# Optimization experiments

Hardware: AMD Instinct MI355X
Metric: run time of the kernel (lower is better)

## Reference

```python
import jax, jax.numpy as jnp
import numpy as np
from jax import lax

P_BOX, N_PTS, K_MAX, HID, SAMP = 512, 50000, 64, 256, 4
C_IMG, HF, WF = 96, 160, 512
IMG_W, IMG_H = 1280.0, 384.0
OFFSET_SCALE = 0.04
PT_IN = 7


def _lin(key, fan_in, fan_out):
    return jax.random.normal(key, (fan_in, fan_out), dtype=jnp.float32) / np.sqrt(fan_in)


def setup_inputs() -> dict:
    key = jax.random.key(0)
    ks = jax.random.split(key, 24)
    xy = jax.random.uniform(ks[0], (N_PTS, 2), minval=-40.0, maxval=40.0)
    z = jax.random.uniform(ks[1], (N_PTS, 1), minval=-2.0, maxval=4.0)
    feats = jax.random.normal(ks[2], (N_PTS, 4))
    points = jnp.concatenate([xy, z, feats], axis=-1).astype(jnp.float32)
    ctr_xy = jax.random.uniform(ks[3], (P_BOX, 2), minval=-35.0, maxval=35.0)
    ctr_z = jax.random.uniform(ks[4], (P_BOX, 1), minval=-1.0, maxval=2.0)
    dxy = jax.random.uniform(ks[5], (P_BOX, 2), minval=2.0, maxval=6.0)
    dz = jax.random.uniform(ks[6], (P_BOX, 1), minval=1.0, maxval=3.0)
    yaw = jax.random.uniform(ks[7], (P_BOX, 1), minval=-np.pi, maxval=np.pi)
    boxes = jnp.concatenate([ctr_xy, ctr_z, dxy, dz, yaw], axis=-1).astype(jnp.float32)
    image_feat = jax.random.normal(ks[8], (1, C_IMG, HF, WF), dtype=jnp.float32)
    fx = fy = 400.0
    proj = jnp.array([[IMG_W / 2, -fx, 0.0, 0.0], [IMG_H / 2, 0.0, -fy, 0.0], [1.0, 0.0, 0.0, 0.0]], dtype=jnp.float32)
    return {
        'points': points, 'boxes': boxes, 'image_feat': image_feat, 'proj': proj,
        'pe_w1': _lin(ks[9], PT_IN + 1, HID), 'pe_b1': jnp.zeros((HID,), jnp.float32),
        'pe_w2': _lin(ks[10], HID, HID), 'pe_b2': jnp.zeros((HID,), jnp.float32),
        'q_w': _lin(ks[11], HID, HID), 'q_b': jnp.zeros((HID,), jnp.float32),
        'f_w': _lin(ks[12], C_IMG, HID), 'f_b': jnp.zeros((HID,), jnp.float32),
        'off_w': _lin(ks[13], HID, SAMP * 2), 'off_b': jnp.zeros((SAMP * 2,), jnp.float32),
        'wt_w': _lin(ks[14], HID, SAMP), 'wt_b': jnp.zeros((SAMP,), jnp.float32),
        'o_w1': _lin(ks[15], 2 * HID, HID), 'o_b1': jnp.zeros((HID,), jnp.float32),
        'o_w2': _lin(ks[16], HID, HID), 'o_b2': jnp.zeros((HID,), jnp.float32),
        'score_w': _lin(ks[17], HID, 1), 'score_b': jnp.zeros((1,), jnp.float32),
    }


def _fused_features(points, boxes, image_feat, proj, pe_w1, pe_b1, pe_w2, pe_b2,
                    q_w, q_b, f_w, f_b, off_w, off_b, wt_w, wt_b,
                    o_w1, o_b1, o_w2, o_b2, score_w, score_b):
    NEG = jnp.float32(-1e30)
    xyz = points[:, :3]
    ctr, dims, yaw = boxes[:, :3], boxes[:, 3:6], boxes[:, 6]
    c, s = jnp.cos(yaw)[:, None], jnp.sin(yaw)[:, None]
    rel = xyz[None, :, :] - ctr[:, None, :]                      # [P,N,3]
    lx = rel[..., 0] * c + rel[..., 1] * s                       # box-frame coords
    ly = -rel[..., 0] * s + rel[..., 1] * c
    lz = rel[..., 2]
    half = dims[:, None, :] * 0.5
    inside = (jnp.abs(lx) <= half[..., 0]) & (jnp.abs(ly) <= half[..., 1]) & (jnp.abs(lz) <= half[..., 2])
    counts = inside.sum(axis=1)                                  # [P]
    d = jnp.maximum(dims, 1e-3)[:, None, :]
    nx, ny, nz = lx / d[..., 0], ly / d[..., 1], lz / d[..., 2] - 0.5
    planar = jnp.where(inside, jnp.sqrt(nx * nx + ny * ny), jnp.inf)
    _, idx = lax.top_k(-planar, K_MAX)                           # K closest inside points
    slot_valid = jnp.arange(K_MAX)[None, :] < counts[:, None]    # [P,K]
    take = lambda a: jnp.take_along_axis(a, idx, axis=1)
    nl = jnp.stack([take(nx), take(ny), take(nz)], axis=-1)      # [P,K,3]
    nl = jnp.where(slot_valid[..., None], nl, 0.0)
    pts_sel = jnp.where(slot_valid[..., None], points[idx], 0.0)  # [P,K,7]
    # local density: knn(4) mean distance, excluding self
    diff = nl[:, :, None, :] - nl[:, None, :, :]
    dmat = jnp.sqrt((diff * diff).sum(-1) + 1e-12)               # [P,K,K]
    dmat = jnp.where(slot_valid[:, None, :], dmat, jnp.inf)
    knn = -lax.top_k(-dmat, 4)[0]                                # 4 smallest, col0 = self
    m = jnp.minimum(counts, K_MAX)
    col_ok = jnp.arange(1, 4)[None, None, :] < jnp.minimum(m, 4)[:, None, None]
    nb = jnp.where(col_ok, knn[:, :, 1:], 0.0)
    n_nb = jnp.maximum(jnp.minimum(m, 4) - 1, 1).astype(nl.dtype)
    density = jnp.where(slot_valid, jnp.exp(-nb.sum(-1) / n_nb[:, None]), 0.0)  # [P,K]
    tokens = jnp.concatenate([nl, pts_sel[:, :, 3:PT_IN], density[..., None]], axis=-1)  # [P,K,8]
    h = jnp.maximum(tokens @ pe_w1 + pe_b1, 0.0) @ pe_w2 + pe_b2  # point encoder [P,K,H]
    # project points to normalized image coords
    hom = pts_sel[:, :, :3] @ proj[:, :3].T + proj[:, 3]
    depth = hom[..., 2]
    safe_d = jnp.where(jnp.abs(depth) > 1e-3, depth, 1e-3)
    rx = 2.0 * (hom[..., 0] / safe_d) / (IMG_W - 1.0) - 1.0
    ry = 2.0 * (hom[..., 1] / safe_d) / (IMG_H - 1.0) - 1.0
    ref = jnp.stack([rx, ry], axis=-1)                           # [P,K,2]
    valid = (depth > 0.1) & (jnp.abs(rx) <= 1.0) & (jnp.abs(ry) <= 1.0) & slot_valid
    # cross-modal deformable attention (lite)
    q = h @ q_w + q_b
    fm = jnp.einsum('chw,cd->dhw', image_feat[0], f_w) + f_b[:, None, None]  # [H,Hf,Wf]
    offs = (jnp.tanh(h @ off_w + off_b)).reshape(P_BOX, K_MAX, SAMP, 2) * OFFSET_SCALE
    w = jax.nn.softmax(h @ wt_w + wt_b, axis=-1)                 # [P,K,S]
    grid = jnp.clip(ref[:, :, None, :] + offs, -1.2, 1.2)
    px = (grid[..., 0] + 1.0) * 0.5 * (WF - 1)                   # align_corners=True
    py = (grid[..., 1] + 1.0) * 0.5 * (HF - 1)
    x0, y0 = jnp.floor(px), jnp.floor(py)

    def gather(xi, yi):
        inb = (xi >= 0) & (xi <= WF - 1) & (yi >= 0) & (yi <= HF - 1)
        xc = jnp.clip(xi, 0, WF - 1).astype(jnp.int32)
        yc = jnp.clip(yi, 0, HF - 1).astype(jnp.int32)
        return fm[:, yc, xc] * inb[None].astype(fm.dtype)        # [H,P,K,S]

    wx1, wy1 = px - x0, py - y0
    samp = (gather(x0, y0) * (1 - wx1) * (1 - wy1) + gather(x0 + 1, y0) * wx1 * (1 - wy1)
            + gather(x0, y0 + 1) * (1 - wx1) * wy1 + gather(x0 + 1, y0 + 1) * wx1 * wy1)
    samp = jnp.moveaxis(samp, 0, -1)                             # [P,K,S,H]
    vm = valid.astype(h.dtype)
    samp = samp * vm[:, :, None, None]
    w = w * vm[:, :, None]
    w = w / jnp.maximum(w.sum(-1, keepdims=True), 1e-6)
    context = (samp * w[..., None]).sum(axis=2) * vm[..., None]  # [P,K,H]
    cat = jnp.concatenate([q * vm[..., None], context], axis=-1)
    img_tok = jnp.maximum(cat @ o_w1 + o_b1, 0.0) @ o_w2 + o_b2
    fused = h + img_tok                                          # [P,K,H]
    # masked attention pooling over valid slots
    logits = (fused @ score_w + score_b).squeeze(-1)
    logits = jnp.where(slot_valid, logits, NEG)
    valid_rows = slot_valid.any(axis=1)
    logits = jnp.where(valid_rows[:, None], logits, 0.0)
    pw = jnp.where(valid_rows[:, None], jax.nn.softmax(logits, axis=-1), 0.0)
    pooled = jnp.einsum('pk,pkd->pd', pw, fused)                 # [P,H]
    return pooled, counts.astype(jnp.float32)[:, None]


def reference(points, boxes, image_feat, proj, pe_w1, pe_b1, pe_w2, pe_b2,
              q_w, q_b, f_w, f_b, off_w, off_b, wt_w, wt_b,
              o_w1, o_b1, o_w2, o_b2, score_w, score_b):
    return _fused_features(points, boxes, image_feat, proj, pe_w1, pe_b1, pe_w2, pe_b2,
                           q_w, q_b, f_w, f_b, off_w, off_b, wt_w, wt_b,
                           o_w1, o_b1, o_w2, o_b2, score_w, score_b)
```

## Files before the change

### kernel.cpp

```cpp
#include <hip/hip_runtime.h>
#include <hip/hip_bf16.h>

#define P_BOX 512
#define NP    50000
#define NPAD  50176
#define KM    64
#define NKEY  4096
#define HF    160
#define WF    512

typedef unsigned long long u64;
typedef unsigned short u16;
typedef unsigned int u32;
typedef __attribute__((ext_vector_type(8))) short short8;
typedef __attribute__((ext_vector_type(4))) float f32x4;

__device__ __forceinline__ u16 f2bf(float f) {
  u32 u = __float_as_uint(f);
  u32 r = u + 0x7fffu + ((u >> 16) & 1u);
  return (u16)(r >> 16);
}
__device__ __forceinline__ float bf2f(u16 h) { return __uint_as_float(((u32)h) << 16); }
__device__ __forceinline__ float bfl(u32 u) { return __uint_as_float(u << 16); }
__device__ __forceinline__ float bfh(u32 u) { return __uint_as_float(u & 0xffff0000u); }

__device__ __forceinline__ int aIdx(int m, int d) {
  return m * 256 + (((d >> 3) ^ (m & 7)) << 3) + (d & 7);
}
__device__ __forceinline__ const short8* aGr(const u16* A, int m, int g) {
  return (const short8*)(A + m * 256 + ((g ^ (m & 7)) << 3));
}
__device__ __forceinline__ u16* aGrW(u16* A, int m, int g) {
  return A + m * 256 + ((g ^ (m & 7)) << 3);
}

__launch_bounds__(256, 4)
__global__ void k_prep(const float* __restrict__ pts,
                       const float* __restrict__ img,
                       const float* __restrict__ q_w, const float* __restrict__ q_b,
                       const float* __restrict__ f_w, const float* __restrict__ f_b,
                       const float* __restrict__ o_w1, const float* __restrict__ pe_w2,
                       const float* __restrict__ o_w2, const float* __restrict__ off_w,
                       const float* __restrict__ wt_w, const float* __restrict__ off_b,
                       const float* __restrict__ wt_b,
                       float* __restrict__ xs, float* __restrict__ ys, float* __restrict__ zs,
                       u16* __restrict__ pe_w2T, u16* __restrict__ WqT,
                       u16* __restrict__ o_w2T, u16* __restrict__ FoT,
                       u16* __restrict__ HWT, float* __restrict__ bq,
                       float* __restrict__ fbo, float* __restrict__ hb,
                       u16* __restrict__ imgT) {
  __shared__ float shbuf[8580];
  const int blk = blockIdx.x;
  const int t = threadIdx.x;

  if (blk < 24) {
    const bool isWq = blk < 16;
    const int g = isWq ? blk : blk - 16;
    const int n0 = (g & 3) * 64;
    const int x0 = (g >> 2) * 64;
    float* sA = shbuf;
    float* sB = shbuf + 64 * 65;
    float acc[4][4];
#pragma unroll
    for (int r = 0; r < 4; ++r)
#pragma unroll
      for (int c = 0; c < 4; ++c) acc[r][c] = 0.f;
    const int tx = t & 15, ty = t >> 4;
    for (int j0 = 0; j0 < 256; j0 += 64) {
      {
        int nn = t & 63;
        int jb = t >> 6;
#pragma unroll
        for (int r = 0; r < 16; ++r) {
          int jj = jb + r * 4;
          int row = (isWq ? 0 : 256) + j0 + jj;
          sA[jj * 65 + nn] = o_w1[row * 256 + n0 + nn];
        }
      }
      {
        int jj = t & 63;
        int xb = t >> 6;
#pragma unroll
        for (int r = 0; r < 16; ++r) {
          int xx = xb + r * 4;
          float v = 0.f;
          if (isWq) v = q_w[(x0 + xx) * 256 + j0 + jj];
          else if (x0 + xx < 96) v = f_w[(x0 + xx) * 256 + j0 + jj];
          sB[jj * 65 + xx] = v;
        }
      }
      __syncthreads();
#pragma unroll 8
      for (int jj = 0; jj < 64; ++jj) {
        float a[4], b[4];
#pragma unroll
        for (int r = 0; r < 4; ++r) a[r] = sA[jj * 65 + ty * 4 + r];
#pragma unroll
        for (int c = 0; c < 4; ++c) b[c] = sB[jj * 65 + tx * 4 + c];
#pragma unroll
        for (int r = 0; r < 4; ++r)
#pragma unroll
          for (int c = 0; c < 4; ++c) acc[r][c] += a[r] * b[c];
      }
      __syncthreads();
    }
    if (isWq) {
#pragma unroll
      for (int r = 0; r < 4; ++r) {
        ushort4 o;
        o.x = f2bf(acc[r][0]); o.y = f2bf(acc[r][1]);
        o.z = f2bf(acc[r][2]); o.w = f2bf(acc[r][3]);
        *(ushort4*)(WqT + (size_t)(n0 + ty * 4 + r) * 256 + x0 + tx * 4) = o;
      }
    } else {
      if (x0 + tx * 4 < 96) {
#pragma unroll
        for (int r = 0; r < 4; ++r) {
          ushort4 o;
          o.x = f2bf(acc[r][0]); o.y = f2bf(acc[r][1]);
          o.z = f2bf(acc[r][2]); o.w = f2bf(acc[r][3]);
          *(ushort4*)(FoT + (size_t)(n0 + ty * 4 + r) * 96 + x0 + tx * 4) = o;
        }
      }
    }
  } else if (blk < 56) {
    int g = blk - 24;
    const float* src = (g < 16) ? pe_w2 : o_w2;
    u16* dst = (g < 16) ? pe_w2T : o_w2T;
    int tile = g & 15;
    int n0 = (tile & 3) * 64, k0 = (tile >> 2) * 64;
    {
      int nn = t & 63, kb = t >> 6;
#pragma unroll
      for (int r = 0; r < 16; ++r) {
        int kk = kb + r * 4;
        shbuf[kk * 65 + nn] = src[(k0 + kk) * 256 + n0 + nn];
      }
    }
    __syncthreads();
    {
      int kk = t & 63, nb = t >> 6;
#pragma unroll
      for (int r = 0; r < 16; ++r) {
        int nn = nb + r * 4;
        dst[(size_t)(n0 + nn) * 256 + k0 + kk] = f2bf(shbuf[kk * 65 + nn]);
      }
    }
  } else if (blk == 56) {
    int n = t;
    float a1 = 0.f, a2 = 0.f;
    for (int j = 0; j < 256; ++j) {
      a1 += q_b[j] * o_w1[j * 256 + n];
      a2 += f_b[j] * o_w1[(256 + j) * 256 + n];
    }
    bq[n] = a1;
    fbo[n] = a2;
#pragma unroll
    for (int s = 0; s < 16; ++s) {
      float v = (s < 8) ? off_w[n * 8 + s] : ((s < 12) ? wt_w[n * 4 + (s - 8)] : 0.f);
      HWT[s * 256 + n] = f2bf(v);
    }
    if (t < 16) hb[t] = (t < 8) ? off_b[t] : ((t < 12) ? wt_b[t - 8] : 0.f);
  } else if (blk < 1337) {
    int g = blk - 57;
    int w0 = (g & 7) * 64;
    int h = g >> 3;
    int c0 = t >> 6, w = t & 63;
    for (int it = 0; it < 24; ++it) {
      int c = it * 4 + c0;
      shbuf[c * 65 + w] = img[(c * HF + h) * WF + w0 + w];
    }
    __syncthreads();
    for (int it = 0; it < 24; ++it) {
      int idx = it * 256 + t;
      int ww = idx / 96, c = idx % 96;
      imgT[((size_t)(h * WF + w0 + ww)) * 96 + c] = f2bf(shbuf[c * 65 + ww]);
    }
  } else {
    int g = blk - 1337;
#pragma unroll
    for (int r = 0; r < 4; ++r) {
      int i = g * 1024 + r * 256 + t;
      if (i < NPAD) {
        if (i < NP) {
          xs[i] = pts[i * 7 + 0];
          ys[i] = pts[i * 7 + 1];
          zs[i] = pts[i * 7 + 2];
        } else {
          xs[i] = 1e9f; ys[i] = 1e9f; zs[i] = 1e9f;
        }
      }
    }
  }
}

__launch_bounds__(512, 4)
__global__ void k_main(const float* __restrict__ pts, const float* __restrict__ boxes,
                       const float* __restrict__ proj,
                       const float* __restrict__ pe_w1, const float* __restrict__ pe_b1,
                       const float* __restrict__ pe_b2,
                       const float* __restrict__ o_b1, const float* __restrict__ o_b2,
                       const float* __restrict__ score_w, const float* __restrict__ score_b,
                       const float* __restrict__ xs, const float* __restrict__ ys,
                       const float* __restrict__ zs,
                       const u16* __restrict__ pe_w2T, const u16* __restrict__ WqT,
                       const u16* __restrict__ o_w2T, const u16* __restrict__ FoT,
                       const u16* __restrict__ HWT,
                       const float* __restrict__ bqv, const float* __restrict__ fbov,
                       const float* __restrict__ hbv,
                       const u16* __restrict__ imgT, float* __restrict__ out) {
  __shared__ __align__(16) char smem[81920];
  u16* A1 = (u16*)smem;
  u16* A2 = (u16*)(smem + 32768);
  u16* CTX = (u16*)(smem + 65536);
  float* poolf = (float*)(smem + 65536);
  float* s_nl = poolf;
  float* s_xyz = poolf + 192;
  float* s_ft = poolf + 384;
  float* s_tok = poolf + 640;
  float* s_vm = (float*)(smem + 77824);
  float* s_coef = s_vm + 64;
  float* s_wl = s_coef + 64;
  float* s_ref = s_wl + 256;
  float* s_lg = s_ref + 128;
  float* s_pw = s_lg + 64;
  u16* s_offb = (u16*)(s_pw + 64);
  int* cntp = (int*)(s_offb + 512);
  u64* keys = (u64*)smem;
  u64* keys2 = (u64*)(smem + 32768);
  float* s_knn = (float*)(smem + 32768 + 1024);

  const int p = blockIdx.x;
  const int tid = threadIdx.x;

  const float cx = boxes[p * 7 + 0], cy = boxes[p * 7 + 1], cz = boxes[p * 7 + 2];
  const float dx = boxes[p * 7 + 3], dy = boxes[p * 7 + 4], dz = boxes[p * 7 + 5];
  const float yaw = boxes[p * 7 + 6];
  const float cth = cosf(yaw), sth = sinf(yaw);
  const float hx = dx * 0.5f, hy = dy * 0.5f, hz = dz * 0.5f;
  const float ddx = fmaxf(dx, 1e-3f), ddy = fmaxf(dy, 1e-3f), ddz = fmaxf(dz, 1e-3f);

  if (tid == 0) *cntp = 0;
  __syncthreads();

  for (int i = tid * 4; i < NPAD; i += 2048) {
    float4 x4 = *(const float4*)(xs + i);
    float4 y4 = *(const float4*)(ys + i);
    float4 z4 = *(const float4*)(zs + i);
#pragma unroll
    for (int c = 0; c < 4; ++c) {
      float xv = (c == 0) ? x4.x : (c == 1) ? x4.y : (c == 2) ? x4.z : x4.w;
      float yv = (c == 0) ? y4.x : (c == 1) ? y4.y : (c == 2) ? y4.z : y4.w;
      float zv = (c == 0) ? z4.x : (c == 1) ? z4.y : (c == 2) ? z4.z : z4.w;
      float rx0 = xv - cx, ry0 = yv - cy, rz0 = zv - cz;
      float lx = rx0 * cth + ry0 * sth;
      float ly = ry0 * cth - rx0 * sth;
      if (fabsf(lx) <= hx && fabsf(ly) <= hy && fabsf(rz0) <= hz) {
        int pos = atomicAdd(cntp, 1);
        if (pos < NKEY) {
          float nx = lx / ddx, ny = ly / ddy;
          float pl = sqrtf(nx * nx + ny * ny);
          keys[pos] = (((u64)__float_as_uint(pl)) << 32) | (u32)(i + c);
        }
      }
    }
  }
  __syncthreads();
  const int cnt = *cntp;
  const int m = min(cnt, KM);

  if (cnt <= KM) {
    if (tid < cnt) keys2[tid] = keys[tid];
  } else {
    int cc = min(cnt, NKEY);
    if (cc <= 1024) {
      u64 k0v = ~0ull, k1v = ~0ull;
      bool h0 = tid < cc, h1 = tid + 512 < cc;
      if (h0) k0v = keys[tid];
      if (h1) k1v = keys[tid + 512];
      int r0 = 0, r1 = 0;
      for (int i = 0; i < cc; ++i) {
        u64 ki = keys[i];
        r0 += (ki < k0v) ? 1 : 0;
        r1 += (ki < k1v) ? 1 : 0;
      }
      if (h0 && r0 < KM) keys2[r0] = k0v;
      if (h1 && r1 < KM) keys2[r1] = k1v;
    } else {
      int nn = 2048;
      while (nn < cc) nn <<= 1;
      for (int i = cc + tid; i < nn; i += 512) keys[i] = ~0ull;
      __syncthreads();
      for (int k = 2; k <= nn; k <<= 1) {
        for (int j = k >> 1; j > 0; j >>= 1) {
          for (int t = tid; t < nn; t += 512) {
            int ixj = t ^ j;
            if (ixj > t) {
              u64 a = keys[t], b = keys[ixj];
              bool up = ((t & k) == 0);
              if ((a > b) == up) { keys[t] = b; keys[ixj] = a; }
            }
          }
          __syncthreads();
        }
      }
      if (tid < KM) keys2[tid] = keys[tid];
    }
  }
  __syncthreads();

  if (tid < KM) {
    int k = tid;
    float x = 0.f, y = 0.f, z = 0.f, n0 = 0.f, n1 = 0.f, n2 = 0.f;
    float f0 = 0.f, f1 = 0.f, f2 = 0.f, f3 = 0.f;
    if (k < m) {
      u32 pi = (u32)(keys2[k] & 0xffffffffu);
      const float* pp = pts + (size_t)pi * 7;
      x = pp[0]; y = pp[1]; z = pp[2];
      f0 = pp[3]; f1 = pp[4]; f2 = pp[5]; f3 = pp[6];
      float rx0 = x - cx, ry0 = y - cy, rz0 = z - cz;
      float lx = rx0 * cth + ry0 * sth;
      float ly = ry0 * cth - rx0 * sth;
      n0 = lx / ddx; n1 = ly / ddy; n2 = rz0 / ddz - 0.5f;
    }
    s_nl[k * 3 + 0] = n0; s_nl[k * 3 + 1] = n1; s_nl[k * 3 + 2] = n2;
    s_xyz[k * 3 + 0] = x; s_xyz[k * 3 + 1] = y; s_xyz[k * 3 + 2] = z;
    s_ft[k * 4 + 0] = f0; s_ft[k * 4 + 1] = f1; s_ft[k * 4 + 2] = f2; s_ft[k * 4 + 3] = f3;
    float h0 = proj[0] * x + proj[1] * y + proj[2] * z + proj[3];
    float h1 = proj[4] * x + proj[5] * y + proj[6] * z + proj[7];
    float dep = proj[8] * x + proj[9] * y + proj[10] * z + proj[11];
    float sd = (fabsf(dep) > 1e-3f) ? dep : 1e-3f;
    float rx = 2.f * (h0 / sd) / 1279.f - 1.f;
    float ry = 2.f * (h1 / sd) / 383.f - 1.f;
    bool v = (dep > 0.1f) && (fabsf(rx) <= 1.f) && (fabsf(ry) <= 1.f) && (k < m);
    s_vm[k] = v ? 1.f : 0.f;
    s_ref[k * 2 + 0] = rx;
    s_ref[k * 2 + 1] = ry;
  }
  __syncthreads();

  {
    int k = tid & 63, part = tid >> 6;
    float a0 = s_nl[k * 3], a1 = s_nl[k * 3 + 1], a2 = s_nl[k * 3 + 2];
    float b0 = 1e30f, b1 = 1e30f, b2 = 1e30f, b3 = 1e30f;
#pragma unroll
    for (int jj = 0; jj < 8; ++jj) {
      int j = part * 8 + jj;
      if (j < m) {
        float d0 = a0 - s_nl[j * 3], d1 = a1 - s_nl[j * 3 + 1], d2 = a2 - s_nl[j * 3 + 2];
        float dd = sqrtf(d0 * d0 + d1 * d1 + d2 * d2 + 1e-12f);
        if (dd < b3) {
          if (dd < b0)      { b3 = b2; b2 = b1; b1 = b0; b0 = dd; }
          else if (dd < b1) { b3 = b2; b2 = b1; b1 = dd; }
          else if (dd < b2) { b3 = b2; b2 = dd; }
          else              { b3 = dd; }
        }
      }
    }
    float* o = s_knn + k * 32 + part * 4;
    o[0] = b0; o[1] = b1; o[2] = b2; o[3] = b3;
  }
  __syncthreads();

  if (tid < KM) {
    int k = tid;
    float dens = 0.f;
    if (k < m) {
      float b0 = 1e30f, b1 = 1e30f, b2 = 1e30f, b3 = 1e30f;
#pragma unroll
      for (int i = 0; i < 32; ++i) {
        float dd = s_knn[k * 32 + i];
        if (dd < b3) {
          if (dd < b0)      { b3 = b2; b2 = b1; b1 = b0; b0 = dd; }
          else if (dd < b1) { b3 = b2; b2 = b1; b1 = dd; }
          else if (dd < b2) { b3 = b2; b2 = dd; }
          else              { b3 = dd; }
        }
      }
      int mm = min(m, 4);
      float nbs = 0.f;
      if (mm > 1) nbs += b1;
      if (mm > 2) nbs += b2;
      if (mm > 3) nbs += b3;
      dens = expf(-nbs / (float)max(mm - 1, 1));
    }
    s_tok[k * 8 + 0] = s_nl[k * 3 + 0];
    s_tok[k * 8 + 1] = s_nl[k * 3 + 1];
    s_tok[k * 8 + 2] = s_nl[k * 3 + 2];
    s_tok[k * 8 + 3] = s_ft[k * 4 + 0];
    s_tok[k * 8 + 4] = s_ft[k * 4 + 1];
    s_tok[k * 8 + 5] = s_ft[k * 4 + 2];
    s_tok[k * 8 + 6] = s_ft[k * 4 + 3];
    s_tok[k * 8 + 7] = dens;
  }
  __syncthreads();

  const int wv = tid >> 6, lane = tid & 63, q = lane >> 4, ln = lane & 15;
  const int n0g = wv * 32;

  {
    int k = tid >> 3, d0 = (tid & 7) * 32;
    float acc[32];
    const float4* bp = (const float4*)(pe_b1 + d0);
#pragma unroll
    for (int c4 = 0; c4 < 8; ++c4) {
      float4 b = bp[c4];
      acc[c4 * 4 + 0] = b.x; acc[c4 * 4 + 1] = b.y; acc[c4 * 4 + 2] = b.z; acc[c4 * 4 + 3] = b.w;
    }
#pragma unroll
    for (int j = 0; j < 8; ++j) {
      float tj = s_tok[k * 8 + j];
      const float4* wr = (const float4*)(pe_w1 + j * 256 + d0);
#pragma unroll
      for (int c4 = 0; c4 < 8; ++c4) {
        float4 w = wr[c4];
        acc[c4 * 4 + 0] += tj * w.x; acc[c4 * 4 + 1] += tj * w.y;
        acc[c4 * 4 + 2] += tj * w.z; acc[c4 * 4 + 3] += tj * w.w;
      }
    }
#pragma unroll
    for (int gi = 0; gi < 4; ++gi) {
      u32 pk0 = (u32)f2bf(fmaxf(acc[gi * 8 + 0], 0.f)) | ((u32)f2bf(fmaxf(acc[gi * 8 + 1], 0.f)) << 16);
      u32 pk1 = (u32)f2bf(fmaxf(acc[gi * 8 + 2], 0.f)) | ((u32)f2bf(fmaxf(acc[gi * 8 + 3], 0.f)) << 16);
      u32 pk2 = (u32)f2bf(fmaxf(acc[gi * 8 + 4], 0.f)) | ((u32)f2bf(fmaxf(acc[gi * 8 + 5], 0.f)) << 16);
      u32 pk3 = (u32)f2bf(fmaxf(acc[gi * 8 + 6], 0.f)) | ((u32)f2bf(fmaxf(acc[gi * 8 + 7], 0.f)) << 16);
      uint4 pk = make_uint4(pk0, pk1, pk2, pk3);
      *(uint4*)aGrW(A1, k, (d0 >> 3) + gi) = pk;
    }
  }
  __syncthreads();

  {
    f32x4 acc[4][2];
#pragma unroll
    for (int mt = 0; mt < 4; ++mt) { acc[mt][0] = (f32x4)0.f; acc[mt][1] = (f32x4)0.f; }
    const u16* B0 = pe_w2T + (size_t)(n0g + ln) * 256 + q * 8;
    const u16* B1 = B0 + 16 * 256;
#pragma unroll
    for (int ks = 0; ks < 8; ++ks) {
      short8 b0 = *(const short8*)(B0 + ks * 32);
      short8 b1 = *(const short8*)(B1 + ks * 32);
#pragma unroll
      for (int mt = 0; mt < 4; ++mt) {
        short8 af = *aGr(A1, ln + 16 * mt, ks * 4 + q);
        acc[mt][0] = __builtin_amdgcn_mfma_f32_16x16x32_bf16(af, b0, acc[mt][0], 0, 0, 0);
        acc[mt][1] = __builtin_amdgcn_mfma_f32_16x16x32_bf16(af, b1, acc[mt][1], 0, 0, 0);
      }
    }
    float bias0 = pe_b2[n0g + ln], bias1 = pe_b2[n0g + 16 + ln];
#pragma unroll
    for (int mt = 0; mt < 4; ++mt)
#pragma unroll
      for (int r = 0; r < 4; ++r) {
        int mm = mt * 16 + q * 4 + r;
        A2[aIdx(mm, n0g + ln)] = f2bf(acc[mt][0][r] + bias0);
        A2[aIdx(mm, n0g + 16 + ln)] = f2bf(acc[mt][1][r] + bias1);
      }
  }
  __syncthreads();

  if (wv < 4) {
    f32x4 acc = (f32x4)0.f;
    const u16* B = HWT + (size_t)ln * 256 + q * 8;
#pragma unroll
    for (int ks = 0; ks < 8; ++ks) {
      short8 af = *aGr(A2, ln + 16 * wv, ks * 4 + q);
      short8 b = *(const short8*)(B + ks * 32);
      acc = __builtin_amdgcn_mfma_f32_16x16x32_bf16(af, b, acc, 0, 0, 0);
    }
    float hb_ = hbv[ln];
#pragma unroll
    for (int r = 0; r < 4; ++r) {
      int mm = wv * 16 + q * 4 + r;
      float val = acc[r] + hb_;
      if (ln < 8) s_offb[mm * 8 + ln] = f2bf(tanhf(val) * 0.04f);
      else if (ln < 12) s_wl[mm * 4 + (ln - 8)] = val;
    }
  }
  __syncthreads();

  if (tid < KM) {
    int k = tid;
    float l0 = s_wl[k * 4], l1 = s_wl[k * 4 + 1], l2 = s_wl[k * 4 + 2], l3 = s_wl[k * 4 + 3];
    float mx = fmaxf(fmaxf(l0, l1), fmaxf(l2, l3));
    float e0 = expf(l0 - mx), e1 = expf(l1 - mx), e2 = expf(l2 - mx), e3 = expf(l3 - mx);
    float si = 1.f / (e0 + e1 + e2 + e3);
    s_wl[k * 4] = e0 * si; s_wl[k * 4 + 1] = e1 * si;
    s_wl[k * 4 + 2] = e2 * si; s_wl[k * 4 + 3] = e3 * si;
  }
  __syncthreads();

  {
    int k = tid >> 3, cg = tid & 7;
    float acc[12];
#pragma unroll
    for (int c = 0; c < 12; ++c) acc[c] = 0.f;
    float coef_ = 0.f;
    if (s_vm[k] > 0.f) {
      float rx = s_ref[k * 2], ry = s_ref[k * 2 + 1];
#pragma unroll
      for (int s = 0; s < 4; ++s) {
        float ox = bf2f(s_offb[k * 8 + s * 2]), oy = bf2f(s_offb[k * 8 + s * 2 + 1]);
        float gx = fminf(fmaxf(rx + ox, -1.2f), 1.2f);
        float gy = fminf(fmaxf(ry + oy, -1.2f), 1.2f);
        float px = (gx + 1.f) * 0.5f * 511.f;
        float py = (gy + 1.f) * 0.5f * 159.f;
        float x0f = floorf(px), y0f = floorf(py);
        float wx1 = px - x0f, wy1 = py - y0f;
        float ws_ = s_wl[k * 4 + s];
        int x0 = (int)x0f, y0 = (int)y0f;
#pragma unroll
        for (int t2 = 0; t2 < 4; ++t2) {
          int xi = x0 + (t2 & 1), yi = y0 + (t2 >> 1);
          if (xi >= 0 && xi <= WF - 1 && yi >= 0 && yi <= HF - 1) {
            float tw = ((t2 & 1) ? wx1 : 1.f - wx1) * ((t2 >> 1) ? wy1 : 1.f - wy1);
            float w2 = ws_ * tw;
            coef_ += w2;
            const u16* pp = imgT + ((size_t)(yi * WF + xi)) * 96 + cg * 12;
            uint2 u0 = *(const uint2*)pp;
            uint2 u1 = *(const uint2*)(pp + 4);
            uint2 u2 = *(const uint2*)(pp + 8);
            acc[0] += w2 * bfl(u0.x); acc[1] += w2 * bfh(u0.x);
            acc[2] += w2 * bfl(u0.y); acc[3] += w2 * bfh(u0.y);
            acc[4] += w2 * bfl(u1.x); acc[5] += w2 * bfh(u1.x);
            acc[6] += w2 * bfl(u1.y); acc[7] += w2 * bfh(u1.y);
            acc[8] += w2 * bfl(u2.x); acc[9] += w2 * bfh(u2.x);
            acc[10] += w2 * bfl(u2.y); acc[11] += w2 * bfh(u2.y);
          }
        }
      }
    }
    u16* cp = CTX + k * 96 + cg * 12;
    u32 o0 = (u32)f2bf(acc[0]) | ((u32)f2bf(acc[1]) << 16);
    u32 o1 = (u32)f2bf(acc[2]) | ((u32)f2bf(acc[3]) << 16);
    u32 o2 = (u32)f2bf(acc[4]) | ((u32)f2bf(acc[5]) << 16);
    u32 o3 = (u32)f2bf(acc[6]) | ((u32)f2bf(acc[7]) << 16);
    u32 o4 = (u32)f2bf(acc[8]) | ((u32)f2bf(acc[9]) << 16);
    u32 o5 = (u32)f2bf(acc[10]) | ((u32)f2bf(acc[11]) << 16);
    *(uint2*)cp = make_uint2(o0, o1);
    *(uint2*)(cp + 4) = make_uint2(o2, o3);
    *(uint2*)(cp + 8) = make_uint2(o4, o5);
    if (cg == 0) s_coef[k] = coef_;
  }
  __syncthreads();

  {
#pragma unroll
    for (int nt = 0; nt < 2; ++nt) {
      int n = n0g + nt * 16 + ln;
      f32x4 aB[4];
#pragma unroll
      for (int mt = 0; mt < 4; ++mt) aB[mt] = (f32x4)0.f;
      const u16* BF = FoT + (size_t)n * 96 + q * 8;
#pragma unroll
      for (int ks = 0; ks < 3; ++ks) {
        short8 b = *(const short8*)(BF + ks * 32);
#pragma unroll
        for (int mt = 0; mt < 4; ++mt) {
          short8 cf = *(const short8*)(CTX + (ln + 16 * mt) * 96 + ks * 32 + q * 8);
          aB[mt] = __builtin_amdgcn_mfma_f32_16x16x32_bf16(cf, b, aB[mt], 0, 0, 0);
        }
      }
      f32x4 aA[4];
#pragma unroll
      for (int mt = 0; mt < 4; ++mt) aA[mt] = (f32x4)0.f;
      const u16* BW = WqT + (size_t)n * 256 + q * 8;
#pragma unroll
      for (int ks = 0; ks < 8; ++ks) {
        short8 b = *(const short8*)(BW + ks * 32);
#pragma unroll
        for (int mt = 0; mt < 4; ++mt) {
          short8 af = *aGr(A2, ln + 16 * mt, ks * 4 + q);
          aA[mt] = __builtin_amdgcn_mfma_f32_16x16x32_bf16(af, b, aA[mt], 0, 0, 0);
        }
      }
      float fb = fbov[n], ob = o_b1[n], bq_ = bqv[n];
#pragma unroll
      for (int mt = 0; mt < 4; ++mt)
#pragma unroll
        for (int r = 0; r < 4; ++r) {
          int mm = mt * 16 + q * 4 + r;
          float val = s_vm[mm] * (aA[mt][r] + bq_) + aB[mt][r] + s_coef[mm] * fb + ob;
          A1[aIdx(mm, n)] = f2bf(fmaxf(val, 0.f));
        }
    }
  }
  __syncthreads();

  {
    f32x4 acc[4][2];
#pragma unroll
    for (int mt = 0; mt < 4; ++mt) { acc[mt][0] = (f32x4)0.f; acc[mt][1] = (f32x4)0.f; }
    const u16* B0 = o_w2T + (size_t)(n0g + ln) * 256 + q * 8;
    const u16* B1 = B0 + 16 * 256;
#pragma unroll
    for (int ks = 0; ks < 8; ++ks) {
      short8 b0 = *(const short8*)(B0 + ks * 32);
      short8 b1 = *(const short8*)(B1 + ks * 32);
#pragma unroll
      for (int mt = 0; mt < 4; ++mt) {
        short8 af = *aGr(A1, ln + 16 * mt, ks * 4 + q);
        acc[mt][0] = __builtin_amdgcn_mfma_f32_16x16x32_bf16(af, b0, acc[mt][0], 0, 0, 0);
        acc[mt][1] = __builtin_amdgcn_mfma_f32_16x16x32_bf16(af, b1, acc[mt][1], 0, 0, 0);
      }
    }
    float b20 = o_b2[n0g + ln], b21 = o_b2[n0g + 16 + ln];
#pragma unroll
    for (int mt = 0; mt < 4; ++mt)
#pragma unroll
      for (int r = 0; r < 4; ++r) {
        int mm = mt * 16 + q * 4 + r;
        int i0 = aIdx(mm, n0g + ln), i1 = aIdx(mm, n0g + 16 + ln);
        float fu0 = bf2f(A2[i0]) + acc[mt][0][r] + b20;
        float fu1 = bf2f(A2[i1]) + acc[mt][1][r] + b21;
        A2[i0] = f2bf(fu0);
        A2[i1] = f2bf(fu1);
      }
  }
  __syncthreads();

  {
    int k = tid >> 3, part = tid & 7;
    float a = 0.f;
#pragma unroll
    for (int gi = 0; gi < 4; ++gi) {
      int g = part * 4 + gi;
      uint4 uu = *(const uint4*)aGr(A2, k, g);
      const float4* sw = (const float4*)(score_w + g * 8);
      float4 s0 = sw[0], s1 = sw[1];
      a += bfl(uu.x) * s0.x + bfh(uu.x) * s0.y + bfl(uu.y) * s0.z + bfh(uu.y) * s0.w;
      a += bfl(uu.z) * s1.x + bfh(uu.z) * s1.y + bfl(uu.w) * s1.z + bfh(uu.w) * s1.w;
    }
    poolf[k * 8 + part] = a;
  }
  __syncthreads();
  if (tid < KM) {
    float a = score_b[0];
#pragma unroll
    for (int j = 0; j < 8; ++j) a += poolf[tid * 8 + j];
    s_lg[tid] = a;
  }
  __syncthreads();

  if (wv == 0) {
    int k = lane;
    float lg = (k < m) ? s_lg[k] : -1e30f;
    float mx = lg;
#pragma unroll
    for (int o = 32; o; o >>= 1) mx = fmaxf(mx, __shfl_xor(mx, o));
    float e = (k < m) ? expf(lg - mx) : 0.f;
    float ss = e;
#pragma unroll
    for (int o = 32; o; o >>= 1) ss += __shfl_xor(ss, o);
    s_pw[k] = (m > 0 && k < m) ? e / ss : 0.f;
  }
  __syncthreads();

  if (tid < 256) {
    int d = tid;
    float acc = 0.f;
    for (int k = 0; k < KM; ++k) acc += s_pw[k] * bf2f(A2[aIdx(k, d)]);
    out[(size_t)p * 256 + d] = acc;
  }
  if (tid == 0) out[(size_t)P_BOX * 256 + p] = (float)cnt;
}

extern "C" void kernel_launch(void* const* d_in, const int* in_sizes, int n_in,
                              void* d_out, int out_size, void* d_ws, size_t ws_size,
                              hipStream_t stream) {
  (void)in_sizes; (void)n_in; (void)out_size; (void)ws_size;
  const float* points  = (const float*)d_in[0];
  const float* boxes   = (const float*)d_in[1];
  const float* img     = (const float*)d_in[2];
  const float* proj    = (const float*)d_in[3];
  const float* pe_w1   = (const float*)d_in[4];
  const float* pe_b1   = (const float*)d_in[5];
  const float* pe_w2   = (const float*)d_in[6];
  const float* pe_b2   = (const float*)d_in[7];
  const float* q_w     = (const float*)d_in[8];
  const float* q_b     = (const float*)d_in[9];
  const float* f_w     = (const float*)d_in[10];
  const float* f_b     = (const float*)d_in[11];
  const float* off_w   = (const float*)d_in[12];
  const float* off_b   = (const float*)d_in[13];
  const float* wt_w    = (const float*)d_in[14];
  const float* wt_b    = (const float*)d_in[15];
  const float* o_w1    = (const float*)d_in[16];
  const float* o_b1    = (const float*)d_in[17];
  const float* o_w2    = (const float*)d_in[18];
  const float* o_b2    = (const float*)d_in[19];
  const float* score_w = (const float*)d_in[20];
  const float* score_b = (const float*)d_in[21];
  float* out = (float*)d_out;

  char* W = (char*)d_ws;
  float* xs   = (float*)(W + 0);
  float* ysv  = (float*)(W + 200704);
  float* zsv  = (float*)(W + 401408);
  float* bqv  = (float*)(W + 602112);
  float* fbov = (float*)(W + 603136);
  float* hbv  = (float*)(W + 604160);
  u16* pe_w2T = (u16*)(W + 604416);
  u16* WqT    = (u16*)(W + 735488);
  u16* o_w2T  = (u16*)(W + 866560);
  u16* FoT    = (u16*)(W + 997632);
  u16* HWT    = (u16*)(W + 1046784);
  u16* imgT   = (u16*)(W + 1054976);

  k_prep<<<1386, 256, 0, stream>>>(points, img, q_w, q_b, f_w, f_b, o_w1, pe_w2, o_w2,
                                   off_w, wt_w, off_b, wt_b, xs, ysv, zsv,
                                   pe_w2T, WqT, o_w2T, FoT, HWT, bqv, fbov, hbv, imgT);
  k_main<<<P_BOX, 512, 0, stream>>>(points, boxes, proj, pe_w1, pe_b1, pe_b2, o_b1, o_b2,
                                    score_w, score_b, xs, ysv, zsv, pe_w2T, WqT, o_w2T,
                                    FoT, HWT, bqv, fbov, hbv, imgT, out);
}
```

Baseline: 255.9 us.

## Split prep kernel into weight and image kernels, relax launch bounds

Splits the single heterogeneous prep kernel into one kernel for the weight transposes and bias folds and another for the image transpose and point SoA conversion. The image/points kernel declares a smaller shared buffer (96*65 floats instead of 8580) and a minimum of 2 blocks per multiprocessor rather than 4. k_main's launch bound also drops from 4 to 2 blocks per multiprocessor, which lets the compiler use more registers and avoid spills, at the cost of fewer resident waves. The split adds one kernel launch but keeps the few slow GEMM-like weight blocks out of the many image-transpose blocks.

```diff
diff --git a/kernel.cpp b/kernel.cpp
--- a/kernel.cpp
+++ b/kernel.cpp
@@ -34,21 +34,17 @@
   return A + m * 256 + ((g ^ (m & 7)) << 3);
 }
 
-__launch_bounds__(256, 4)
-__global__ void k_prep(const float* __restrict__ pts,
-                       const float* __restrict__ img,
-                       const float* __restrict__ q_w, const float* __restrict__ q_b,
-                       const float* __restrict__ f_w, const float* __restrict__ f_b,
-                       const float* __restrict__ o_w1, const float* __restrict__ pe_w2,
-                       const float* __restrict__ o_w2, const float* __restrict__ off_w,
-                       const float* __restrict__ wt_w, const float* __restrict__ off_b,
-                       const float* __restrict__ wt_b,
-                       float* __restrict__ xs, float* __restrict__ ys, float* __restrict__ zs,
-                       u16* __restrict__ pe_w2T, u16* __restrict__ WqT,
-                       u16* __restrict__ o_w2T, u16* __restrict__ FoT,
-                       u16* __restrict__ HWT, float* __restrict__ bq,
-                       float* __restrict__ fbo, float* __restrict__ hb,
-                       u16* __restrict__ imgT) {
+__launch_bounds__(256, 2)
+__global__ void k_prep_w(const float* __restrict__ q_w, const float* __restrict__ q_b,
+                         const float* __restrict__ f_w, const float* __restrict__ f_b,
+                         const float* __restrict__ o_w1, const float* __restrict__ pe_w2,
+                         const float* __restrict__ o_w2, const float* __restrict__ off_w,
+                         const float* __restrict__ wt_w, const float* __restrict__ off_b,
+                         const float* __restrict__ wt_b,
+                         u16* __restrict__ pe_w2T, u16* __restrict__ WqT,
+                         u16* __restrict__ o_w2T, u16* __restrict__ FoT,
+                         u16* __restrict__ HWT, float* __restrict__ bq,
+                         float* __restrict__ fbo, float* __restrict__ hb) {
   __shared__ float shbuf[8580];
   const int blk = blockIdx.x;
   const int t = threadIdx.x;
@@ -146,7 +142,7 @@
         dst[(size_t)(n0 + nn) * 256 + k0 + kk] = f2bf(shbuf[kk * 65 + nn]);
       }
     }
-  } else if (blk == 56) {
+  } else {
     int n = t;
     float a1 = 0.f, a2 = 0.f;
     for (int j = 0; j < 256; ++j) {
@@ -161,10 +157,19 @@
       HWT[s * 256 + n] = f2bf(v);
     }
     if (t < 16) hb[t] = (t < 8) ? off_b[t] : ((t < 12) ? wt_b[t - 8] : 0.f);
-  } else if (blk < 1337) {
-    int g = blk - 57;
-    int w0 = (g & 7) * 64;
-    int h = g >> 3;
+  }
+}
+
+__launch_bounds__(256, 2)
+__global__ void k_prep_img(const float* __restrict__ pts, const float* __restrict__ img,
+                           float* __restrict__ xs, float* __restrict__ ys,
+                           float* __restrict__ zs, u16* __restrict__ imgT) {
+  __shared__ float shbuf[96 * 65];
+  const int blk = blockIdx.x;
+  const int t = threadIdx.x;
+  if (blk < 1280) {
+    int w0 = (blk & 7) * 64;
+    int h = blk >> 3;
     int c0 = t >> 6, w = t & 63;
     for (int it = 0; it < 24; ++it) {
       int c = it * 4 + c0;
@@ -177,7 +182,7 @@
       imgT[((size_t)(h * WF + w0 + ww)) * 96 + c] = f2bf(shbuf[c * 65 + ww]);
     }
   } else {
-    int g = blk - 1337;
+    int g = blk - 1280;
 #pragma unroll
     for (int r = 0; r < 4; ++r) {
       int i = g * 1024 + r * 256 + t;
@@ -194,7 +199,7 @@
   }
 }
 
-__launch_bounds__(512, 4)
+__launch_bounds__(512, 2)
 __global__ void k_main(const float* __restrict__ pts, const float* __restrict__ boxes,
                        const float* __restrict__ proj,
                        const float* __restrict__ pe_w1, const float* __restrict__ pe_b1,
@@ -707,9 +712,9 @@
   u16* HWT    = (u16*)(W + 1046784);
   u16* imgT   = (u16*)(W + 1054976);
 
-  k_prep<<<1386, 256, 0, stream>>>(points, img, q_w, q_b, f_w, f_b, o_w1, pe_w2, o_w2,
-                                   off_w, wt_w, off_b, wt_b, xs, ysv, zsv,
-                                   pe_w2T, WqT, o_w2T, FoT, HWT, bqv, fbov, hbv, imgT);
+  k_prep_w<<<57, 256, 0, stream>>>(q_w, q_b, f_w, f_b, o_w1, pe_w2, o_w2, off_w, wt_w,
+                                   off_b, wt_b, pe_w2T, WqT, o_w2T, FoT, HWT, bqv, fbov, hbv);
+  k_prep_img<<<1329, 256, 0, stream>>>(points, img, xs, ysv, zsv, imgT);
   k_main<<<P_BOX, 512, 0, stream>>>(points, boxes, proj, pe_w1, pe_b1, pe_b2, o_b1, o_b2,
                                     score_w, score_b, xs, ysv, zsv, pe_w2T, WqT, o_w2T,
                                     FoT, HWT, bqv, fbov, hbv, imgT, out);
```

New measurement: 283.4 us. 10.7% more time.
